# Optimization experiments

Measured on AMD Instinct MI355X. Metric: run time of the kernel, lower is better.

Reference implementation:

```python
import jax, jax.numpy as jnp
import numpy as np

PATCH = 64      # patch_size
K = 16          # num_patches
UNF_K = 16      # unfold kernel
UNF_S = 8       # unfold stride


def setup_inputs() -> dict:
    key = jax.random.key(0)
    k0, k1, k2 = jax.random.split(key, 3)
    B, C, H, W = 32, 3, 384, 384
    x = jax.random.normal(k0, (B, C, H, W), dtype=jnp.float32)
    # encoder params: Conv2d(3,32,3,s2,p1) -> ReLU -> Conv2d(32,64,3,s2,p1) -> GAP
    w1 = jax.random.normal(k1, (32, 3, 3, 3), dtype=jnp.float32) * 0.1
    b1 = jnp.zeros((32,), dtype=jnp.float32)
    w2 = jax.random.normal(k2, (64, 32, 3, 3), dtype=jnp.float32) * 0.05
    b2 = jnp.zeros((64,), dtype=jnp.float32)
    return {"x": x, "w1": w1, "b1": b1, "w2": w2, "b2": b2}


def _patch_variances(x):
    # torch.var(unfold(x,16,8), dim=1), unbiased, over C*16*16 = 768 elems.
    # Computed via window sums instead of materializing the unfold tensor.
    win = (1, 1, UNF_K, UNF_K)
    st = (1, 1, UNF_S, UNF_S)
    s = jax.lax.reduce_window(x, 0.0, jax.lax.add, win, st, 'VALID')
    s2 = jax.lax.reduce_window(x * x, 0.0, jax.lax.add, win, st, 'VALID')
    s = s.sum(axis=1)    # [B, gh, gw]
    s2 = s2.sum(axis=1)  # [B, gh, gw]
    n = x.shape[1] * UNF_K * UNF_K  # 768
    var = (s2 - s * s / n) / (n - 1)
    return var.reshape(var.shape[0], -1)  # [B, gh*gw], row-major like F.unfold


def _encode(patches, w1, b1, w2, b2):
    # patches: [N, 3, 64, 64] -> [N, 64]
    dn = ('NCHW', 'OIHW', 'NCHW')
    y = jax.lax.conv_general_dilated(patches, w1, (2, 2), [(1, 1), (1, 1)],
                                     dimension_numbers=dn) + b1[None, :, None, None]
    y = jax.nn.relu(y)
    y = jax.lax.conv_general_dilated(y, w2, (2, 2), [(1, 1), (1, 1)],
                                     dimension_numbers=dn) + b2[None, :, None, None]
    return y.mean(axis=(2, 3))  # AdaptiveAvgPool2d(1)


def reference(x, w1, b1, w2, b2):
    B, C, H, W = x.shape
    var = _patch_variances(x)                 # [B, L]
    _, idx = jax.lax.top_k(var, K)            # [B, K]
    # faithful (buggy) decode from the source: divisor is W//8, step 8
    h = (idx // (W // UNF_S)) * UNF_S         # [B, K]
    w = (idx % (W // UNF_S)) * UNF_S          # [B, K]

    def slice_one(img, hh, ww):
        # dynamic_slice clamps starts so the 64x64 crop stays in-bounds
        return jax.lax.dynamic_slice(img, (0, hh, ww), (C, PATCH, PATCH))

    gather = jax.vmap(lambda img, hs, ws: jax.vmap(
        lambda hh, ww: slice_one(img, hh, ww))(hs, ws))
    patches = gather(x, h, w)                 # [B, K, 3, 64, 64]
    feats = _encode(patches.reshape(B * K, C, PATCH, PATCH), w1, b1, w2, b2)
    return feats.reshape(B, K, -1).mean(axis=1)  # [B, 64]
```

## Files before the change

### kernel.cpp

```cpp
#include <hip/hip_runtime.h>
#include <math.h>

#define NB 32
#define GH 47
#define GW 47
#define NWIN (GH*GW)
#define KSEL 16
#define RPITCH 17
#define SEG 48

__global__ __launch_bounds__(256) void k_var(const float* __restrict__ x,
                                             float* __restrict__ var)
{
    __shared__ double hs [3][24][SEG];
    __shared__ double hs2[3][24][SEG];
    int gyp = blockIdx.x;
    int b   = blockIdx.y;
    int tid = threadIdx.x;
    int R0  = gyp * 16;

    for (int tau = tid; tau < 3*24*SEG; tau += 256) {
        int sg = tau % SEG;
        int t2 = tau / SEG;
        int rr = t2 % 24;
        int c  = t2 / 24;
        int row = R0 + rr;
        double s = 0.0, s2 = 0.0;
        if (row < 384) {
            const float* px = x + (((size_t)(b*3 + c)*384 + row)*384 + sg*8);
            #pragma unroll
            for (int q = 0; q < 2; ++q) {
                float4 v = *reinterpret_cast<const float4*>(px + q*4);
                double a0 = v.x, a1 = v.y, a2 = v.z, a3 = v.w;
                s  += a0 + a1 + a2 + a3;
                s2 = fma(a0,a0, fma(a1,a1, fma(a2,a2, fma(a3,a3, s2))));
            }
        }
        hs [c][rr][sg] = s;
        hs2[c][rr][sg] = s2;
    }
    __syncthreads();

    if (tid < 188) {
        int which = tid & 1;
        int rest  = tid >> 1;
        int gx = rest % 47, g = rest / 47;
        int gy = gyp*2 + g;
        if (gy < GH) {
            const double* base = which ? &hs2[0][0][0] : &hs[0][0][0];
            double S = 0.0;
            #pragma unroll
            for (int c = 0; c < 3; ++c)
                #pragma unroll
                for (int r = 0; r < 16; ++r) {
                    const double* rp = base + ((c*24) + (g*8 + r))*SEG + gx;
                    S += rp[0] + rp[1];
                }
            double P = __shfl_xor(S, 1, 64);
            if (which == 0) {
                var[(size_t)b*NWIN + gy*GW + gx] =
                    (float)((P - S*S/768.0) / 767.0);
            }
        }
    }
}

__global__ __launch_bounds__(512, 2) void k_encode(const float* __restrict__ x,
    const float* __restrict__ w1, const float* __restrict__ b1,
    const float* __restrict__ var, float* __restrict__ sbuf)
{
    __shared__ float4 sin4[3*66*RPITCH];
    __shared__ float  s_part[8][2][8][3];
    __shared__ float  s_c31[4][8][3];
    __shared__ int    s_hw[2];

    int p     = blockIdx.x;
    int bimg  = p >> 4;
    int krank = p & 15;
    int tid   = threadIdx.x;

    if (tid < 64) {
        int l = tid;
        const float* vb = var + (size_t)bimg*NWIN;
        unsigned long long key[35];
        #pragma unroll
        for (int j = 0; j < 35; ++j) {
            int idx = j*64 + l;
            unsigned long long kk = 0ULL;
            if (idx < NWIN) {
                unsigned u = __float_as_uint(vb[idx]);
                unsigned mono = u ^ ((unsigned)((int)u >> 31) | 0x80000000u);
                kk = ((unsigned long long)mono << 12) | (unsigned)(4095 - idx);
            }
            key[j] = kk;
        }
        unsigned long long bk = 0ULL;
        for (int it = 0; ; ++it) {
            bk = 0ULL;
            #pragma unroll
            for (int j = 0; j < 35; ++j) bk = key[j] > bk ? key[j] : bk;
            #pragma unroll
            for (int m = 1; m < 64; m <<= 1) {
                unsigned long long o = __shfl_xor(bk, m, 64);
                bk = o > bk ? o : bk;
            }
            if (it == krank) break;
            #pragma unroll
            for (int j = 0; j < 35; ++j) if (key[j] == bk) key[j] = 0ULL;
        }
        if (l == 0) {
            int idx = 4095 - (int)(bk & 0xFFFULL);
            int h = (idx / 48) * 8; if (h > 320) h = 320;
            int w = (idx % 48) * 8; if (w > 320) w = 320;
            s_hw[0] = h; s_hw[1] = w;
        }
    } else {
        float4 z4 = make_float4(0.f, 0.f, 0.f, 0.f);
        for (int i = tid - 64; i < 3*66*RPITCH; i += 448) sin4[i] = z4;
    }
    __syncthreads();

    int h0 = s_hw[0];
    int w0 = s_hw[1];

    float* sinf = (float*)sin4;
    #pragma unroll
    for (int it = 0; it < 6; ++it) {
        int fi  = tid + it*512;
        int c   = fi >> 10;
        int rem = fi & 1023;
        int y   = rem >> 4;
        int x4  = rem & 15;
        float4 v = *reinterpret_cast<const float4*>(
            x + (((size_t)(bimg*3 + c)*384 + (h0 + y))*384 + w0 + x4*4));
        int r  = y + 1;
        int sw = (r >> 1) & 7;
        float vals[4] = {v.x, v.y, v.z, v.w};
        #pragma unroll
        for (int e = 0; e < 4; ++e) {
            int pcol = x4*4 + 1 + e;
            int k  = pcol >> 2, bb = pcol & 3;
            int ks = (k < 16) ? ((k & 8) | ((k & 7) ^ sw)) : 16;
            sinf[((c*66 + r)*RPITCH + ks)*4 + bb] = vals[e];
        }
    }
    __syncthreads();

    int wave = tid >> 6;
    int lane = tid & 63;
    int sub  = wave & 1;
    int icg  = __builtin_amdgcn_readfirstlane(tid >> 7);
    int iy   = sub*16 + (lane >> 2);
    int xq   = lane & 3;

    float acc[8][8];
    #pragma unroll
    for (int i = 0; i < 8; ++i)
        #pragma unroll
        for (int u = 0; u < 8; ++u) acc[i][u] = 0.f;

    const float* w1g = w1 + icg*8*27;

    for (int ch = 0; ch < 3; ++ch) {
        for (int ky = 0; ky < 3; ++ky) {
            int r    = 2*iy + ky;
            int sw   = (r >> 1) & 7;
            int base = (ch*66 + r)*RPITCH;
            float s[17];
            #pragma unroll
            for (int j = 0; j < 4; ++j) {
                int k = 4*xq + j;
                float4 v = sin4[base + ((k & 8) | ((k & 7) ^ sw))];
                s[4*j+0] = v.x; s[4*j+1] = v.y; s[4*j+2] = v.z; s[4*j+3] = v.w;
            }
            {
                int k  = 4*xq + 4;
                int ks = (k < 16) ? ((k & 8) | ((k & 7) ^ sw)) : 16;
                s[16] = sinf[(base + ks)*4];
            }
            const float* wp = w1g + ch*9 + ky*3;
            #pragma unroll
            for (int i = 0; i < 8; ++i) {
                float wA = wp[i*27 + 0];
                float wB = wp[i*27 + 1];
                float wC = wp[i*27 + 2];
                #pragma unroll
                for (int u = 0; u < 8; ++u)
                    acc[i][u] = fmaf(s[2*u], wA,
                                 fmaf(s[2*u+1], wB,
                                  fmaf(s[2*u+2], wC, acc[i][u])));
            }
        }
    }

    float R[8][3];
    #pragma unroll
    for (int i = 0; i < 8; ++i) {
        float bias = b1[icg*8 + i];
        float c1 = 0.f, c2 = 0.f, v7 = 0.f;
        #pragma unroll
        for (int u = 0; u < 8; ++u) {
            float v = fmaxf(acc[i][u] + bias, 0.f);
            if (u & 1) c2 += v; else c1 += v;
            if (u == 7) v7 = v;
        }
        R[i][0] = c2 - ((xq == 3) ? v7 : 0.f);
        R[i][1] = c1;
        R[i][2] = c2;
    }

    #pragma unroll
    for (int m = 1; m <= 2; m <<= 1)
        #pragma unroll
        for (int i = 0; i < 8; ++i)
            #pragma unroll
            for (int k = 0; k < 3; ++k)
                R[i][k] += __shfl_xor(R[i][k], m, 64);

    float c31[8][3];
    #pragma unroll
    for (int i = 0; i < 8; ++i)
        #pragma unroll
        for (int k = 0; k < 3; ++k)
            c31[i][k] = __shfl(R[i][k], 60, 64);

    #pragma unroll
    for (int m = 8; m < 64; m <<= 1)
        #pragma unroll
        for (int i = 0; i < 8; ++i)
            #pragma unroll
            for (int k = 0; k < 3; ++k)
                R[i][k] += __shfl_xor(R[i][k], m, 64);

    if (lane == 0) {
        #pragma unroll
        for (int i = 0; i < 8; ++i)
            #pragma unroll
            for (int k = 0; k < 3; ++k)
                s_part[wave][0][i][k] = R[i][k];
    } else if (lane == 4) {
        #pragma unroll
        for (int i = 0; i < 8; ++i)
            #pragma unroll
            for (int k = 0; k < 3; ++k)
                s_part[wave][1][i][k] = R[i][k];
    }
    if (sub == 1 && lane == 8) {
        #pragma unroll
        for (int i = 0; i < 8; ++i)
            #pragma unroll
            for (int k = 0; k < 3; ++k)
                s_c31[icg][i][k] = c31[i][k];
    }
    __syncthreads();

    if (tid < 288) {
        int ic = tid / 9, j = tid - ic*9;
        int ky = j / 3, kx = j - ky*3;
        int g = ic >> 3, i = ic & 7;
        float even = s_part[2*g][0][i][kx] + s_part[2*g+1][0][i][kx];
        float odd  = s_part[2*g][1][i][kx] + s_part[2*g+1][1][i][kx];
        float val = (ky == 1) ? even : odd;
        if (ky == 0) val = odd - s_c31[g][i][kx];
        sbuf[(size_t)p*288 + tid] = val;
    }
}

__global__ __launch_bounds__(256) void k_reduce(const float* __restrict__ sbuf,
    const float* __restrict__ w2, const float* __restrict__ b2,
    float* __restrict__ out)
{
    __shared__ float Ssum[288];
    __shared__ float s_part[256];
    int b = blockIdx.x, tid = threadIdx.x;

    for (int i = tid; i < 288; i += 256) {
        float s = 0.f;
        #pragma unroll
        for (int k = 0; k < KSEL; ++k)
            s += sbuf[(size_t)(b*KSEL + k)*288 + i];
        Ssum[i] = s;
    }
    __syncthreads();

    int oc = tid & 63, q = tid >> 6;
    const float4* w4 = reinterpret_cast<const float4*>(w2 + oc*288 + q*72);
    const float4* S4 = reinterpret_cast<const float4*>(Ssum + q*72);
    float a = 0.f;
    #pragma unroll
    for (int t = 0; t < 18; ++t) {
        float4 wv = w4[t];
        float4 sv = S4[t];
        a = fmaf(wv.x, sv.x, fmaf(wv.y, sv.y,
             fmaf(wv.z, sv.z, fmaf(wv.w, sv.w, a))));
    }
    s_part[tid] = a;
    __syncthreads();
    if (tid < 64) {
        float t = s_part[tid] + s_part[64 + tid] + s_part[128 + tid] + s_part[192 + tid];
        out[b*64 + tid] = b2[tid] + t * (1.0f/4096.0f);
    }
}

extern "C" void kernel_launch(void* const* d_in, const int* in_sizes, int n_in,
                              void* d_out, int out_size, void* d_ws, size_t ws_size,
                              hipStream_t stream)
{
    const float* x  = (const float*)d_in[0];
    const float* w1 = (const float*)d_in[1];
    const float* b1 = (const float*)d_in[2];
    const float* w2 = (const float*)d_in[3];
    const float* b2 = (const float*)d_in[4];
    float* out = (float*)d_out;

    char* ws = (char*)d_ws;
    float* var  = (float*)ws;
    float* sbuf = (float*)(ws + 283904);

    k_var   <<<dim3(24, NB), 256, 0, stream>>>(x, var);
    k_encode<<<NB*KSEL,      512, 0, stream>>>(x, w1, b1, var, sbuf);
    k_reduce<<<NB,           256, 0, stream>>>(sbuf, w2, b2, out);
}
```

Measured before the change: 77.29 us.

## Split top-k selection into its own kernel and zero only padding halo

The top-k selection previously ran redundantly in every one of the 512 encode blocks, each iterating up to its rank. Now a separate kernel with one 64-thread wave per image computes all 16 coordinates once and writes them to workspace, and the encode blocks just read their coordinates. The shared-memory clear is also narrowed from the whole input tile to only the top padding row and left padding column. This removes repeated selection work and a serial phase at the start of each encode block, at the cost of an extra kernel launch with only 32 small blocks.

```diff
diff --git a/kernel.cpp b/kernel.cpp
--- a/kernel.cpp
+++ b/kernel.cpp
@@ -65,65 +65,69 @@
     }
 }
 
-__global__ __launch_bounds__(512, 2) void k_encode(const float* __restrict__ x,
-    const float* __restrict__ w1, const float* __restrict__ b1,
-    const float* __restrict__ var, float* __restrict__ sbuf)
-{
-    __shared__ float4 sin4[3*66*RPITCH];
-    __shared__ float  s_part[8][2][8][3];
-    __shared__ float  s_c31[4][8][3];
-    __shared__ int    s_hw[2];
-
-    int p     = blockIdx.x;
-    int bimg  = p >> 4;
-    int krank = p & 15;
-    int tid   = threadIdx.x;
-
-    if (tid < 64) {
-        int l = tid;
-        const float* vb = var + (size_t)bimg*NWIN;
-        unsigned long long key[35];
-        #pragma unroll
-        for (int j = 0; j < 35; ++j) {
-            int idx = j*64 + l;
-            unsigned long long kk = 0ULL;
-            if (idx < NWIN) {
-                unsigned u = __float_as_uint(vb[idx]);
-                unsigned mono = u ^ ((unsigned)((int)u >> 31) | 0x80000000u);
-                kk = ((unsigned long long)mono << 12) | (unsigned)(4095 - idx);
-            }
-            key[j] = kk;
-        }
+__global__ void k_sel(const float* __restrict__ var, int* __restrict__ coords)
+{
+    int b = blockIdx.x, l = threadIdx.x;
+    unsigned long long key[35];
+    #pragma unroll
+    for (int j = 0; j < 35; ++j) {
+        int idx = j*64 + l;
+        unsigned long long kk = 0ULL;
+        if (idx < NWIN) {
+            unsigned u = __float_as_uint(var[(size_t)b*NWIN + idx]);
+            unsigned mono = u ^ ((unsigned)((int)u >> 31) | 0x80000000u);
+            kk = ((unsigned long long)mono << 12) | (unsigned)(4095 - idx);
+        }
+        key[j] = kk;
+    }
+    for (int it = 0; it < KSEL; ++it) {
         unsigned long long bk = 0ULL;
-        for (int it = 0; ; ++it) {
-            bk = 0ULL;
-            #pragma unroll
-            for (int j = 0; j < 35; ++j) bk = key[j] > bk ? key[j] : bk;
-            #pragma unroll
-            for (int m = 1; m < 64; m <<= 1) {
-                unsigned long long o = __shfl_xor(bk, m, 64);
-                bk = o > bk ? o : bk;
-            }
-            if (it == krank) break;
-            #pragma unroll
-            for (int j = 0; j < 35; ++j) if (key[j] == bk) key[j] = 0ULL;
-        }
+        #pragma unroll
+        for (int j = 0; j < 35; ++j) bk = key[j] > bk ? key[j] : bk;
+        #pragma unroll
+        for (int m = 1; m < 64; m <<= 1) {
+            unsigned long long o = __shfl_xor(bk, m, 64);
+            bk = o > bk ? o : bk;
+        }
+        #pragma unroll
+        for (int j = 0; j < 35; ++j) if (key[j] == bk) key[j] = 0ULL;
         if (l == 0) {
             int idx = 4095 - (int)(bk & 0xFFFULL);
             int h = (idx / 48) * 8; if (h > 320) h = 320;
             int w = (idx % 48) * 8; if (w > 320) w = 320;
-            s_hw[0] = h; s_hw[1] = w;
-        }
-    } else {
-        float4 z4 = make_float4(0.f, 0.f, 0.f, 0.f);
-        for (int i = tid - 64; i < 3*66*RPITCH; i += 448) sin4[i] = z4;
-    }
-    __syncthreads();
-
-    int h0 = s_hw[0];
-    int w0 = s_hw[1];
+            coords[(b*KSEL + it)*2 + 0] = h;
+            coords[(b*KSEL + it)*2 + 1] = w;
+        }
+    }
+}
+
+__global__ __launch_bounds__(512, 2) void k_encode(const float* __restrict__ x,
+    const float* __restrict__ w1, const float* __restrict__ b1,
+    const int* __restrict__ coords, float* __restrict__ sbuf)
+{
+    __shared__ float4 sin4[3*66*RPITCH];
+    __shared__ float  s_part[8][2][8][3];
+    __shared__ float  s_c31[4][8][3];
+
+    int p    = blockIdx.x;
+    int bimg = p >> 4;
+    int tid  = threadIdx.x;
+    int h0 = coords[p*2 + 0];
+    int w0 = coords[p*2 + 1];
 
     float* sinf = (float*)sin4;
+
+    if (tid < 243) {
+        int c = tid / 81, j = tid - c*81;
+        if (j < 17) {
+            sin4[(c*66 + 0)*RPITCH + j] = make_float4(0.f, 0.f, 0.f, 0.f);
+        } else {
+            int r  = j - 16;
+            int sw = (r >> 1) & 7;
+            sinf[((c*66 + r)*RPITCH + sw)*4] = 0.f;
+        }
+    }
+
     #pragma unroll
     for (int it = 0; it < 6; ++it) {
         int fi  = tid + it*512;
@@ -314,10 +318,12 @@
     float* out = (float*)d_out;
 
     char* ws = (char*)d_ws;
-    float* var  = (float*)ws;
-    float* sbuf = (float*)(ws + 283904);
+    int*   coords = (int*)ws;
+    float* var    = (float*)(ws + 4096);
+    float* sbuf   = (float*)(ws + 287744);
 
     k_var   <<<dim3(24, NB), 256, 0, stream>>>(x, var);
-    k_encode<<<NB*KSEL,      512, 0, stream>>>(x, w1, b1, var, sbuf);
+    k_sel   <<<NB,            64, 0, stream>>>(var, coords);
+    k_encode<<<NB*KSEL,      512, 0, stream>>>(x, w1, b1, coords, sbuf);
     k_reduce<<<NB,           256, 0, stream>>>(sbuf, w2, b2, out);
 }
```

Measured after the change: 74.11 us. 1.04x faster.
